# Optimization experiments

Measured on AMD Instinct MI355X. Metric: run time of the kernel, lower is better.

Reference implementation:

```python
import jax, jax.numpy as jnp
import numpy as np

N_NODES = 100000
N_EDGES = 1600000
IN_FEATS = 64
NUM_CLASSES = 64


def setup_inputs() -> dict:
    key = jax.random.key(0)
    k1, k2, k3, k4, k5, k6 = jax.random.split(key, 6)
    in_feat = jax.random.normal(k1, (N_NODES, IN_FEATS), dtype=jnp.float32)
    src = jax.random.randint(k2, (N_EDGES,), 0, N_NODES, dtype=jnp.int32)
    dst = jax.random.randint(k3, (N_EDGES,), 0, N_NODES, dtype=jnp.int32)
    scale = 1.0 / np.sqrt(IN_FEATS)
    W_self = jax.random.normal(k4, (IN_FEATS, NUM_CLASSES), dtype=jnp.float32) * scale
    W_neigh = jax.random.normal(k5, (IN_FEATS, NUM_CLASSES), dtype=jnp.float32) * scale
    bias = jax.random.normal(k6, (NUM_CLASSES,), dtype=jnp.float32) * 0.01
    return {"in_feat": in_feat, "src": src, "dst": dst,
            "W_self": W_self, "W_neigh": W_neigh, "bias": bias}


def reference(in_feat, src, dst, W_self, W_neigh, bias):
    # SAGEConv with 'mean' aggregator (DGL semantics):
    #   h_neigh[v] = mean over incoming edges (u->v) of in_feat[u]; 0 if no in-edges
    #   out = fc_self(x) + fc_neigh(h_neigh) + bias, then sigmoid
    n = in_feat.shape[0]
    msg = in_feat[src]                                            # [E, F] gather
    agg = jax.ops.segment_sum(msg, dst, num_segments=n)           # [N, F]
    deg = jax.ops.segment_sum(jnp.ones((src.shape[0],), jnp.float32), dst,
                              num_segments=n)                     # [N]
    h_neigh = agg / jnp.maximum(deg, 1.0)[:, None]                # mean, 0 for isolated
    out = in_feat @ W_self + h_neigh @ W_neigh + bias
    return jax.nn.sigmoid(out)
```

## Files before the change

kernel.cpp:

```cpp
#include <hip/hip_runtime.h>


constexpr int NN = 100000;
constexpr int NE = 1600000;
constexpr int F  = 64;
constexpr int RB = 256;
constexpr int NB = (NN + RB - 1) / RB;
constexpr int CH = 8192;
constexpr int PB = (NE + CH - 1) / CH;
constexpr int CAP = 2048;

typedef short bf16x8 __attribute__((ext_vector_type(8)));
typedef float f32x4  __attribute__((ext_vector_type(4)));
typedef float f32x2  __attribute__((ext_vector_type(2)));
typedef unsigned short u16;
typedef u16 u16x8 __attribute__((ext_vector_type(8)));

__device__ __forceinline__ u16 f2bf(float f) {
    unsigned u = __float_as_uint(f);
    unsigned r = (u + 0x7FFF + ((u >> 16) & 1)) >> 16;
    return (u16)r;
}

__global__ __launch_bounds__(256) void k_prep(const float* __restrict__ x,
                                              const float* __restrict__ Ws,
                                              const float* __restrict__ Wn,
                                              unsigned char* __restrict__ x8,
                                              u16* __restrict__ xb,
                                              u16* __restrict__ Bt) {
    const int i = blockIdx.x * 256 + threadIdx.x;
    if (i < NN * F / 8) {
        const int o = i * 8;
        float4 a = *(const float4*)&x[o];
        float4 b = *(const float4*)&x[o + 4];
        int lo = 0, hi = 0;
        lo = __builtin_amdgcn_cvt_pk_fp8_f32(a.x, a.y, lo, false);
        lo = __builtin_amdgcn_cvt_pk_fp8_f32(a.z, a.w, lo, true);
        hi = __builtin_amdgcn_cvt_pk_fp8_f32(b.x, b.y, hi, false);
        hi = __builtin_amdgcn_cvt_pk_fp8_f32(b.z, b.w, hi, true);
        *(int2*)&x8[o] = make_int2(lo, hi);
        u16x8 r;
        r[0] = f2bf(a.x); r[1] = f2bf(a.y); r[2] = f2bf(a.z); r[3] = f2bf(a.w);
        r[4] = f2bf(b.x); r[5] = f2bf(b.y); r[6] = f2bf(b.z); r[7] = f2bf(b.w);
        *(u16x8*)&xb[o] = r;
    } else if (i < NN * F / 8 + 1024) {
        const int j  = i - NN * F / 8;
        const int n  = j >> 4;
        const int kb = (j & 15) * 8;
        u16x8 r;
#pragma unroll
        for (int jj = 0; jj < 8; ++jj) {
            const int kk = kb + jj;
            const float w = (kk < 64) ? Ws[kk * 64 + n] : Wn[(kk - 64) * 64 + n];
            r[jj] = f2bf(w);
        }
        *(u16x8*)&Bt[n * 128 + kb] = r;
    }
}

__global__ __launch_bounds__(256) void k_hist(const int* __restrict__ dst,
                                              int* __restrict__ gcount) {
    __shared__ int h[NB];
    for (int i = threadIdx.x; i < NB; i += 256) h[i] = 0;
    __syncthreads();
    const int b0  = blockIdx.x * CH;
    const int end = min(b0 + CH, NE);
    for (int i = b0 + threadIdx.x * 4; i < end; i += 1024) {
        int4 d = *(const int4*)&dst[i];
        atomicAdd(&h[d.x >> 8], 1);
        atomicAdd(&h[d.y >> 8], 1);
        atomicAdd(&h[d.z >> 8], 1);
        atomicAdd(&h[d.w >> 8], 1);
    }
    __syncthreads();
    for (int i = threadIdx.x; i < NB; i += 256)
        if (h[i]) atomicAdd(&gcount[i], h[i]);
}

__global__ __launch_bounds__(512) void k_scan(const int* __restrict__ gcount,
                                              int* __restrict__ basep,
                                              int* __restrict__ cursor) {
    __shared__ int tmp[512];
    const int t = threadIdx.x;
    int val = (t < NB) ? gcount[t] : 0;
    tmp[t] = val;
    __syncthreads();
    int s = val;
    for (int o = 1; o < 512; o <<= 1) {
        int add = (t >= o) ? tmp[t - o] : 0;
        __syncthreads();
        s += add;
        tmp[t] = s;
        __syncthreads();
    }
    if (t < NB) {
        basep[t]  = s - val;
        cursor[t] = s - val;
    }
}

__global__ __launch_bounds__(512) void k_part(const int* __restrict__ src,
                                              const int* __restrict__ dst,
                                              int* __restrict__ cursor,
                                              unsigned* __restrict__ packed) {
    __shared__ unsigned stage[CH];
    __shared__ unsigned short bkt[CH];
    __shared__ int hist[NB], lscan[NB], lcur[NB], gpos[NB];
    __shared__ int tmp[512];

    const int t   = threadIdx.x;
    const int b0  = blockIdx.x * CH;
    const int cnt = min(CH, NE - b0);

    for (int i = t; i < NB; i += 512) hist[i] = 0;
    __syncthreads();

    int4 sv[4], dv[4];
#pragma unroll
    for (int j = 0; j < 4; ++j) {
        const int idx = j * 2048 + t * 4;
        if (idx < cnt) {
            sv[j] = *(const int4*)&src[b0 + idx];
            dv[j] = *(const int4*)&dst[b0 + idx];
            atomicAdd(&hist[dv[j].x >> 8], 1);
            atomicAdd(&hist[dv[j].y >> 8], 1);
            atomicAdd(&hist[dv[j].z >> 8], 1);
            atomicAdd(&hist[dv[j].w >> 8], 1);
        }
    }
    __syncthreads();

    int val = (t < NB) ? hist[t] : 0;
    tmp[t] = val;
    __syncthreads();
    int s = val;
    for (int o = 1; o < 512; o <<= 1) {
        int add = (t >= o) ? tmp[t - o] : 0;
        __syncthreads();
        s += add;
        tmp[t] = s;
        __syncthreads();
    }
    if (t < NB) {
        lscan[t] = s - val;
        lcur[t]  = s - val;
        gpos[t]  = val ? atomicAdd(&cursor[t], val) : 0;
    }
    __syncthreads();

#pragma unroll
    for (int j = 0; j < 4; ++j) {
        const int idx = j * 2048 + t * 4;
        if (idx < cnt) {
            const int ss[4] = {sv[j].x, sv[j].y, sv[j].z, sv[j].w};
            const int dd[4] = {dv[j].x, dv[j].y, dv[j].z, dv[j].w};
#pragma unroll
            for (int q = 0; q < 4; ++q) {
                const int b = dd[q] >> 8;
                const int p = atomicAdd(&lcur[b], 1);
                stage[p] = ((unsigned)(dd[q] & 255) << 17) | (unsigned)ss[q];
                bkt[p]   = (unsigned short)b;
            }
        }
    }
    __syncthreads();

    for (int i = t; i < cnt; i += 512) {
        const int b = bkt[i];
        packed[gpos[b] + (i - lscan[b])] = stage[i];
    }
}

__device__ __forceinline__ void acc8pk(f32x2& a0, f32x2& a1, f32x2& a2, f32x2& a3,
                                       int2 qq) {
#if __has_builtin(__builtin_amdgcn_cvt_pk_f32_fp8)
    a0 += __builtin_amdgcn_cvt_pk_f32_fp8(qq.x, false);
    a1 += __builtin_amdgcn_cvt_pk_f32_fp8(qq.x, true);
    a2 += __builtin_amdgcn_cvt_pk_f32_fp8(qq.y, false);
    a3 += __builtin_amdgcn_cvt_pk_f32_fp8(qq.y, true);
#else
    a0[0] += __builtin_amdgcn_cvt_f32_fp8(qq.x, 0);
    a0[1] += __builtin_amdgcn_cvt_f32_fp8(qq.x, 1);
    a1[0] += __builtin_amdgcn_cvt_f32_fp8(qq.x, 2);
    a1[1] += __builtin_amdgcn_cvt_f32_fp8(qq.x, 3);
    a2[0] += __builtin_amdgcn_cvt_f32_fp8(qq.y, 0);
    a2[1] += __builtin_amdgcn_cvt_f32_fp8(qq.y, 1);
    a3[0] += __builtin_amdgcn_cvt_f32_fp8(qq.y, 2);
    a3[1] += __builtin_amdgcn_cvt_f32_fp8(qq.y, 3);
#endif
}

__global__ __launch_bounds__(512) void k_fused(
    const unsigned char* __restrict__ x8, const u16* __restrict__ xb,
    const unsigned* __restrict__ packed, const int* __restrict__ basep,
    const u16* __restrict__ Bt, const float* __restrict__ bias,
    float* __restrict__ out)
{
    __shared__ u16 At[64 * 128];
    __shared__ unsigned stage[CAP];
    __shared__ int hist[64], cur[64], exar[64];

    const int blk  = blockIdx.x;
    const int base = blk * 64;
    const int bu   = blk >> 2;
    const int qq   = blk & 3;
    const int t    = threadIdx.x;
    const int nv   = min(64, NN - base);

    const int e0 = basep[bu];
    const int e1 = (bu == NB - 1) ? NE : basep[bu + 1];
    const int m  = e1 - e0;

    if (t < 64) hist[t] = 0;
    __syncthreads();

    for (int i = t; i < m; i += 512) {
        const unsigned p  = packed[e0 + i];
        const unsigned dl = p >> 17;
        if ((int)(dl >> 6) == qq) atomicAdd(&hist[dl & 63], 1);
    }
    __syncthreads();

    if (t < 64) {
        const int val = hist[t];
        int s = val;
#pragma unroll
        for (int o = 1; o < 64; o <<= 1) {
            const int nsh = __shfl_up(s, o);
            if (t >= o) s += nsh;
        }
        cur[t]  = s - val;
        exar[t] = s - val;
    }
    __syncthreads();

    for (int i = t; i < m; i += 512) {
        const unsigned p  = packed[e0 + i];
        const unsigned dl = p >> 17;
        if ((int)(dl >> 6) == qq) {
            const int pos = atomicAdd(&cur[dl & 63], 1);
            if (pos < CAP) stage[pos] = p & 0x1FFFFu;
        }
    }
    __syncthreads();

    const int r  = t >> 3;
    const int cg = t & 7;
    if (r < nv) {
        const int dg = hist[r];
        const int s0 = exar[r];
        f32x2 a0 = {0.f, 0.f}, a1 = a0, a2 = a0, a3 = a0;
        int e = 0;
        for (; e + 4 <= dg; e += 4) {
            const int i0 = stage[s0 + e + 0];
            const int i1 = stage[s0 + e + 1];
            const int i2 = stage[s0 + e + 2];
            const int i3 = stage[s0 + e + 3];
            int2 q0 = *(const int2*)&x8[(size_t)i0 * F + cg * 8];
            int2 q1 = *(const int2*)&x8[(size_t)i1 * F + cg * 8];
            int2 q2 = *(const int2*)&x8[(size_t)i2 * F + cg * 8];
            int2 q3 = *(const int2*)&x8[(size_t)i3 * F + cg * 8];
            acc8pk(a0, a1, a2, a3, q0);
            acc8pk(a0, a1, a2, a3, q1);
            acc8pk(a0, a1, a2, a3, q2);
            acc8pk(a0, a1, a2, a3, q3);
        }
        for (; e < dg; ++e) {
            int2 q = *(const int2*)&x8[(size_t)stage[s0 + e] * F + cg * 8];
            acc8pk(a0, a1, a2, a3, q);
        }
        const float inv = 1.0f / fmaxf((float)dg, 1.0f);

        u16x8 hb;
        hb[0] = f2bf(a0[0] * inv); hb[1] = f2bf(a0[1] * inv);
        hb[2] = f2bf(a1[0] * inv); hb[3] = f2bf(a1[1] * inv);
        hb[4] = f2bf(a2[0] * inv); hb[5] = f2bf(a2[1] * inv);
        hb[6] = f2bf(a3[0] * inv); hb[7] = f2bf(a3[1] * inv);
        const int bh = (8 + cg) ^ (r & 15);
        *(u16x8*)&At[r * 128 + bh * 8] = hb;

        const int bx = cg ^ (r & 15);
        *(u16x8*)&At[r * 128 + bx * 8] = *(const u16x8*)&xb[(size_t)(base + r) * F + cg * 8];
    }
    __syncthreads();

    const int w    = t >> 6;
    const int lane = t & 63;
    const int tr   = w >> 1;
    if (tr * 16 >= nv) return;
    const int nh   = w & 1;
    const int r16  = lane & 15;
    const int kg   = lane >> 4;

    bf16x8 bf[4][2];
#pragma unroll
    for (int t4 = 0; t4 < 4; ++t4)
#pragma unroll
        for (int uu = 0; uu < 2; ++uu) {
            const int n = (nh * 2 + uu) * 16 + r16;
            bf[t4][uu] = *(const bf16x8*)&Bt[n * 128 + t4 * 32 + kg * 8];
        }
    const float b0 = bias[(nh * 2 + 0) * 16 + r16];
    const float b1 = bias[(nh * 2 + 1) * 16 + r16];

    const int row = tr * 16 + r16;
    bf16x8 a[4];
#pragma unroll
    for (int t4 = 0; t4 < 4; ++t4) {
        const int blk16 = (t4 * 4 + kg) ^ (row & 15);
        a[t4] = *(const bf16x8*)&At[row * 128 + blk16 * 8];
    }

    f32x4 c0 = {0.f, 0.f, 0.f, 0.f}, c1 = c0;
    c0 = __builtin_amdgcn_mfma_f32_16x16x32_bf16(a[0], bf[0][0], c0, 0, 0, 0);
    c0 = __builtin_amdgcn_mfma_f32_16x16x32_bf16(a[1], bf[1][0], c0, 0, 0, 0);
    c0 = __builtin_amdgcn_mfma_f32_16x16x32_bf16(a[2], bf[2][0], c0, 0, 0, 0);
    c0 = __builtin_amdgcn_mfma_f32_16x16x32_bf16(a[3], bf[3][0], c0, 0, 0, 0);
    c1 = __builtin_amdgcn_mfma_f32_16x16x32_bf16(a[0], bf[0][1], c1, 0, 0, 0);
    c1 = __builtin_amdgcn_mfma_f32_16x16x32_bf16(a[1], bf[1][1], c1, 0, 0, 0);
    c1 = __builtin_amdgcn_mfma_f32_16x16x32_bf16(a[2], bf[2][1], c1, 0, 0, 0);
    c1 = __builtin_amdgcn_mfma_f32_16x16x32_bf16(a[3], bf[3][1], c1, 0, 0, 0);

    float* orow = out + (size_t)(base + tr * 16) * 64;
#pragma unroll
    for (int rr = 0; rr < 4; ++rr) {
        const int ro = (kg * 4 + rr) * 64;
        orow[ro + (nh * 2 + 0) * 16 + r16] = 1.0f / (1.0f + __expf(-(c0[rr] + b0)));
        orow[ro + (nh * 2 + 1) * 16 + r16] = 1.0f / (1.0f + __expf(-(c1[rr] + b1)));
    }
}

extern "C" void kernel_launch(void* const* d_in, const int* in_sizes, int n_in,
                              void* d_out, int out_size, void* d_ws, size_t ws_size,
                              hipStream_t stream) {
    const float* x    = (const float*)d_in[0];
    const int*   src  = (const int*)d_in[1];
    const int*   dst  = (const int*)d_in[2];
    const float* Ws   = (const float*)d_in[3];
    const float* Wn   = (const float*)d_in[4];
    const float* bias = (const float*)d_in[5];
    float* out = (float*)d_out;

    unsigned char* x8 = (unsigned char*)d_ws;
    u16* xb     = (u16*)(x8 + (size_t)NN * F);
    u16* Bt     = xb + (size_t)NN * F;
    int* gcount = (int*)(Bt + 64 * 128);
    int* basep  = gcount + NB;
    int* cursor = basep + NB;
    unsigned* packed = (unsigned*)(cursor + NB);

    hipMemsetAsync(gcount, 0, (size_t)NB * sizeof(int), stream);

    k_prep <<<(NN * F / 8 + 1024 + 255) / 256, 256, 0, stream>>>(x, Ws, Wn, x8, xb, Bt);
    k_hist <<<PB, 256, 0, stream>>>(dst, gcount);
    k_scan <<<1, 512, 0, stream>>>(gcount, basep, cursor);
    k_part <<<PB, 512, 0, stream>>>(src, dst, cursor, packed);

    k_fused<<<(NN + 63) / 64, 512, 0, stream>>>(x8, xb, packed, basep, Bt, bias, out);
}
```

Before: 87.74 us.

## Aggregate neighbours via edge-parallel LDS fixed-point atomics instead of per-row CSR

Replaces the histogram, scan and per-destination sort inside the fused kernel with one compaction pass into shared memory. The gather is then done edge-parallel: each 16-lane group handles one edge and adds its decoded fp8 features into a shared int accumulator using fixed-point atomicAdd. This removes a pass over the packed edges and the per-row load imbalance that comes from varying degree. In exchange it adds many LDS atomics and quantizes sums to 16.16 fixed point, which may cost accuracy.

```diff
diff --git a/kernel.cpp b/kernel.cpp
--- a/kernel.cpp
+++ b/kernel.cpp
@@ -9,6 +9,7 @@
 constexpr int CH = 8192;
 constexpr int PB = (NE + CH - 1) / CH;
 constexpr int CAP = 2048;
+constexpr int AST = 68;
 
 typedef short bf16x8 __attribute__((ext_vector_type(8)));
 typedef float f32x4  __attribute__((ext_vector_type(4)));
@@ -20,6 +21,19 @@
     unsigned u = __float_as_uint(f);
     unsigned r = (u + 0x7FFF + ((u >> 16) & 1)) >> 16;
     return (u16)r;
+}
+
+__device__ __forceinline__ void dec4(int q, float* v) {
+#if __has_builtin(__builtin_amdgcn_cvt_pk_f32_fp8)
+    f32x2 lo = __builtin_amdgcn_cvt_pk_f32_fp8(q, false);
+    f32x2 hi = __builtin_amdgcn_cvt_pk_f32_fp8(q, true);
+    v[0] = lo[0]; v[1] = lo[1]; v[2] = hi[0]; v[3] = hi[1];
+#else
+    v[0] = __builtin_amdgcn_cvt_f32_fp8(q, 0);
+    v[1] = __builtin_amdgcn_cvt_f32_fp8(q, 1);
+    v[2] = __builtin_amdgcn_cvt_f32_fp8(q, 2);
+    v[3] = __builtin_amdgcn_cvt_f32_fp8(q, 3);
+#endif
 }
 
 __global__ __launch_bounds__(256) void k_prep(const float* __restrict__ x,
@@ -171,25 +185,6 @@
     }
 }
 
-__device__ __forceinline__ void acc8pk(f32x2& a0, f32x2& a1, f32x2& a2, f32x2& a3,
-                                       int2 qq) {
-#if __has_builtin(__builtin_amdgcn_cvt_pk_f32_fp8)
-    a0 += __builtin_amdgcn_cvt_pk_f32_fp8(qq.x, false);
-    a1 += __builtin_amdgcn_cvt_pk_f32_fp8(qq.x, true);
-    a2 += __builtin_amdgcn_cvt_pk_f32_fp8(qq.y, false);
-    a3 += __builtin_amdgcn_cvt_pk_f32_fp8(qq.y, true);
-#else
-    a0[0] += __builtin_amdgcn_cvt_f32_fp8(qq.x, 0);
-    a0[1] += __builtin_amdgcn_cvt_f32_fp8(qq.x, 1);
-    a1[0] += __builtin_amdgcn_cvt_f32_fp8(qq.x, 2);
-    a1[1] += __builtin_amdgcn_cvt_f32_fp8(qq.x, 3);
-    a2[0] += __builtin_amdgcn_cvt_f32_fp8(qq.y, 0);
-    a2[1] += __builtin_amdgcn_cvt_f32_fp8(qq.y, 1);
-    a3[0] += __builtin_amdgcn_cvt_f32_fp8(qq.y, 2);
-    a3[1] += __builtin_amdgcn_cvt_f32_fp8(qq.y, 3);
-#endif
-}
-
 __global__ __launch_bounds__(512) void k_fused(
     const unsigned char* __restrict__ x8, const u16* __restrict__ xb,
     const unsigned* __restrict__ packed, const int* __restrict__ basep,
@@ -197,8 +192,10 @@
     float* __restrict__ out)
 {
     __shared__ u16 At[64 * 128];
+    __shared__ int agg[64 * AST];
     __shared__ unsigned stage[CAP];
-    __shared__ int hist[64], cur[64], exar[64];
+    __shared__ int deg[64];
+    __shared__ int scnt;
 
     const int blk  = blockIdx.x;
     const int base = blk * 64;
@@ -211,35 +208,40 @@
     const int e1 = (bu == NB - 1) ? NE : basep[bu + 1];
     const int m  = e1 - e0;
 
-    if (t < 64) hist[t] = 0;
+    for (int i = t; i < 64 * AST; i += 512) agg[i] = 0;
+    if (t < 64) deg[t] = 0;
+    if (t == 0) scnt = 0;
     __syncthreads();
 
     for (int i = t; i < m; i += 512) {
-        const unsigned p  = packed[e0 + i];
-        const unsigned dl = p >> 17;
-        if ((int)(dl >> 6) == qq) atomicAdd(&hist[dl & 63], 1);
-    }
-    __syncthreads();
-
-    if (t < 64) {
-        const int val = hist[t];
-        int s = val;
-#pragma unroll
-        for (int o = 1; o < 64; o <<= 1) {
-            const int nsh = __shfl_up(s, o);
-            if (t >= o) s += nsh;
-        }
-        cur[t]  = s - val;
-        exar[t] = s - val;
-    }
-    __syncthreads();
-
-    for (int i = t; i < m; i += 512) {
-        const unsigned p  = packed[e0 + i];
-        const unsigned dl = p >> 17;
-        if ((int)(dl >> 6) == qq) {
-            const int pos = atomicAdd(&cur[dl & 63], 1);
-            if (pos < CAP) stage[pos] = p & 0x1FFFFu;
+        const unsigned p = packed[e0 + i];
+        if ((int)(p >> 23) == qq) {
+            const int pos = atomicAdd(&scnt, 1);
+            if (pos < CAP) stage[pos] = p;
+        }
+    }
+    __syncthreads();
+    const int ns = min(scnt, CAP);
+
+    const int w    = t >> 6;
+    const int lane = t & 63;
+    const int eidx = lane >> 4;
+    const int l16  = lane & 15;
+    for (int g = w * 4; g < ns; g += 32) {
+        const int e = g + eidx;
+        if (e < ns) {
+            const unsigned p = stage[e];
+            const int r = (int)((p >> 17) & 63);
+            const int s = (int)(p & 0x1FFFFu);
+            const int q = *(const int*)&x8[(size_t)s * F + l16 * 4];
+            float v[4];
+            dec4(q, v);
+            const int ab = r * AST + l16 * 4;
+            atomicAdd(&agg[ab + 0], __float2int_rn(v[0] * 65536.f));
+            atomicAdd(&agg[ab + 1], __float2int_rn(v[1] * 65536.f));
+            atomicAdd(&agg[ab + 2], __float2int_rn(v[2] * 65536.f));
+            atomicAdd(&agg[ab + 3], __float2int_rn(v[3] * 65536.f));
+            if (l16 == 0) atomicAdd(&deg[r], 1);
         }
     }
     __syncthreads();
@@ -247,35 +249,11 @@
     const int r  = t >> 3;
     const int cg = t & 7;
     if (r < nv) {
-        const int dg = hist[r];
-        const int s0 = exar[r];
-        f32x2 a0 = {0.f, 0.f}, a1 = a0, a2 = a0, a3 = a0;
-        int e = 0;
-        for (; e + 4 <= dg; e += 4) {
-            const int i0 = stage[s0 + e + 0];
-            const int i1 = stage[s0 + e + 1];
-            const int i2 = stage[s0 + e + 2];
-            const int i3 = stage[s0 + e + 3];
-            int2 q0 = *(const int2*)&x8[(size_t)i0 * F + cg * 8];
-            int2 q1 = *(const int2*)&x8[(size_t)i1 * F + cg * 8];
-            int2 q2 = *(const int2*)&x8[(size_t)i2 * F + cg * 8];
-            int2 q3 = *(const int2*)&x8[(size_t)i3 * F + cg * 8];
-            acc8pk(a0, a1, a2, a3, q0);
-            acc8pk(a0, a1, a2, a3, q1);
-            acc8pk(a0, a1, a2, a3, q2);
-            acc8pk(a0, a1, a2, a3, q3);
-        }
-        for (; e < dg; ++e) {
-            int2 q = *(const int2*)&x8[(size_t)stage[s0 + e] * F + cg * 8];
-            acc8pk(a0, a1, a2, a3, q);
-        }
-        const float inv = 1.0f / fmaxf((float)dg, 1.0f);
-
+        const float inv = (1.0f / 65536.f) / fmaxf((float)deg[r], 1.0f);
         u16x8 hb;
-        hb[0] = f2bf(a0[0] * inv); hb[1] = f2bf(a0[1] * inv);
-        hb[2] = f2bf(a1[0] * inv); hb[3] = f2bf(a1[1] * inv);
-        hb[4] = f2bf(a2[0] * inv); hb[5] = f2bf(a2[1] * inv);
-        hb[6] = f2bf(a3[0] * inv); hb[7] = f2bf(a3[1] * inv);
+#pragma unroll
+        for (int j = 0; j < 8; ++j)
+            hb[j] = f2bf((float)agg[r * AST + cg * 8 + j] * inv);
         const int bh = (8 + cg) ^ (r & 15);
         *(u16x8*)&At[r * 128 + bh * 8] = hb;
 
@@ -284,13 +262,11 @@
     }
     __syncthreads();
 
-    const int w    = t >> 6;
-    const int lane = t & 63;
-    const int tr   = w >> 1;
+    const int tr = w >> 1;
     if (tr * 16 >= nv) return;
-    const int nh   = w & 1;
-    const int r16  = lane & 15;
-    const int kg   = lane >> 4;
+    const int nh  = w & 1;
+    const int r16 = lane & 15;
+    const int kg  = lane >> 4;
 
     bf16x8 bf[4][2];
 #pragma unroll
```

Result: slower. 115.1 us (+31.2%).

## Merge prep, histogram and scan into one kernel; halve bucket rereads in fused

Applied to the files above, without the earlier changes.

Folds the feature-conversion, destination histogram and global prefix scan into one launch: the last histogram block, detected through an atomic completion counter, performs the scan. This removes two kernel launches. The fused aggregation kernel now handles 128 nodes per block instead of 64, so each 256-node bucket's packed edge list is read by two blocks rather than four, and it keeps the edges in registers between the histogram and scatter passes instead of reading them twice. The risks are more register pressure from the 12-entry edge buffer, a larger shared staging area, and two sequential 64-row passes per block.

```diff
diff --git a/kernel.cpp b/kernel.cpp
--- a/kernel.cpp
+++ b/kernel.cpp
@@ -8,7 +8,9 @@
 constexpr int NB = (NN + RB - 1) / RB;
 constexpr int CH = 8192;
 constexpr int PB = (NE + CH - 1) / CH;
-constexpr int CAP = 2048;
+constexpr int PREPB = (NN * F / 8 + 1024 + 255) / 256;
+constexpr int SCAP = 3072;
+constexpr int NP = 12;
 
 typedef short bf16x8 __attribute__((ext_vector_type(8)));
 typedef float f32x4  __attribute__((ext_vector_type(4)));
@@ -20,155 +22,6 @@
     unsigned u = __float_as_uint(f);
     unsigned r = (u + 0x7FFF + ((u >> 16) & 1)) >> 16;
     return (u16)r;
-}
-
-__global__ __launch_bounds__(256) void k_prep(const float* __restrict__ x,
-                                              const float* __restrict__ Ws,
-                                              const float* __restrict__ Wn,
-                                              unsigned char* __restrict__ x8,
-                                              u16* __restrict__ xb,
-                                              u16* __restrict__ Bt) {
-    const int i = blockIdx.x * 256 + threadIdx.x;
-    if (i < NN * F / 8) {
-        const int o = i * 8;
-        float4 a = *(const float4*)&x[o];
-        float4 b = *(const float4*)&x[o + 4];
-        int lo = 0, hi = 0;
-        lo = __builtin_amdgcn_cvt_pk_fp8_f32(a.x, a.y, lo, false);
-        lo = __builtin_amdgcn_cvt_pk_fp8_f32(a.z, a.w, lo, true);
-        hi = __builtin_amdgcn_cvt_pk_fp8_f32(b.x, b.y, hi, false);
-        hi = __builtin_amdgcn_cvt_pk_fp8_f32(b.z, b.w, hi, true);
-        *(int2*)&x8[o] = make_int2(lo, hi);
-        u16x8 r;
-        r[0] = f2bf(a.x); r[1] = f2bf(a.y); r[2] = f2bf(a.z); r[3] = f2bf(a.w);
-        r[4] = f2bf(b.x); r[5] = f2bf(b.y); r[6] = f2bf(b.z); r[7] = f2bf(b.w);
-        *(u16x8*)&xb[o] = r;
-    } else if (i < NN * F / 8 + 1024) {
-        const int j  = i - NN * F / 8;
-        const int n  = j >> 4;
-        const int kb = (j & 15) * 8;
-        u16x8 r;
-#pragma unroll
-        for (int jj = 0; jj < 8; ++jj) {
-            const int kk = kb + jj;
-            const float w = (kk < 64) ? Ws[kk * 64 + n] : Wn[(kk - 64) * 64 + n];
-            r[jj] = f2bf(w);
-        }
-        *(u16x8*)&Bt[n * 128 + kb] = r;
-    }
-}
-
-__global__ __launch_bounds__(256) void k_hist(const int* __restrict__ dst,
-                                              int* __restrict__ gcount) {
-    __shared__ int h[NB];
-    for (int i = threadIdx.x; i < NB; i += 256) h[i] = 0;
-    __syncthreads();
-    const int b0  = blockIdx.x * CH;
-    const int end = min(b0 + CH, NE);
-    for (int i = b0 + threadIdx.x * 4; i < end; i += 1024) {
-        int4 d = *(const int4*)&dst[i];
-        atomicAdd(&h[d.x >> 8], 1);
-        atomicAdd(&h[d.y >> 8], 1);
-        atomicAdd(&h[d.z >> 8], 1);
-        atomicAdd(&h[d.w >> 8], 1);
-    }
-    __syncthreads();
-    for (int i = threadIdx.x; i < NB; i += 256)
-        if (h[i]) atomicAdd(&gcount[i], h[i]);
-}
-
-__global__ __launch_bounds__(512) void k_scan(const int* __restrict__ gcount,
-                                              int* __restrict__ basep,
-                                              int* __restrict__ cursor) {
-    __shared__ int tmp[512];
-    const int t = threadIdx.x;
-    int val = (t < NB) ? gcount[t] : 0;
-    tmp[t] = val;
-    __syncthreads();
-    int s = val;
-    for (int o = 1; o < 512; o <<= 1) {
-        int add = (t >= o) ? tmp[t - o] : 0;
-        __syncthreads();
-        s += add;
-        tmp[t] = s;
-        __syncthreads();
-    }
-    if (t < NB) {
-        basep[t]  = s - val;
-        cursor[t] = s - val;
-    }
-}
-
-__global__ __launch_bounds__(512) void k_part(const int* __restrict__ src,
-                                              const int* __restrict__ dst,
-                                              int* __restrict__ cursor,
-                                              unsigned* __restrict__ packed) {
-    __shared__ unsigned stage[CH];
-    __shared__ unsigned short bkt[CH];
-    __shared__ int hist[NB], lscan[NB], lcur[NB], gpos[NB];
-    __shared__ int tmp[512];
-
-    const int t   = threadIdx.x;
-    const int b0  = blockIdx.x * CH;
-    const int cnt = min(CH, NE - b0);
-
-    for (int i = t; i < NB; i += 512) hist[i] = 0;
-    __syncthreads();
-
-    int4 sv[4], dv[4];
-#pragma unroll
-    for (int j = 0; j < 4; ++j) {
-        const int idx = j * 2048 + t * 4;
-        if (idx < cnt) {
-            sv[j] = *(const int4*)&src[b0 + idx];
-            dv[j] = *(const int4*)&dst[b0 + idx];
-            atomicAdd(&hist[dv[j].x >> 8], 1);
-            atomicAdd(&hist[dv[j].y >> 8], 1);
-            atomicAdd(&hist[dv[j].z >> 8], 1);
-            atomicAdd(&hist[dv[j].w >> 8], 1);
-        }
-    }
-    __syncthreads();
-
-    int val = (t < NB) ? hist[t] : 0;
-    tmp[t] = val;
-    __syncthreads();
-    int s = val;
-    for (int o = 1; o < 512; o <<= 1) {
-        int add = (t >= o) ? tmp[t - o] : 0;
-        __syncthreads();
-        s += add;
-        tmp[t] = s;
-        __syncthreads();
-    }
-    if (t < NB) {
-        lscan[t] = s - val;
-        lcur[t]  = s - val;
-        gpos[t]  = val ? atomicAdd(&cursor[t], val) : 0;
-    }
-    __syncthreads();
-
-#pragma unroll
-    for (int j = 0; j < 4; ++j) {
-        const int idx = j * 2048 + t * 4;
-        if (idx < cnt) {
-            const int ss[4] = {sv[j].x, sv[j].y, sv[j].z, sv[j].w};
-            const int dd[4] = {dv[j].x, dv[j].y, dv[j].z, dv[j].w};
-#pragma unroll
-            for (int q = 0; q < 4; ++q) {
-                const int b = dd[q] >> 8;
-                const int p = atomicAdd(&lcur[b], 1);
-                stage[p] = ((unsigned)(dd[q] & 255) << 17) | (unsigned)ss[q];
-                bkt[p]   = (unsigned short)b;
-            }
-        }
-    }
-    __syncthreads();
-
-    for (int i = t; i < cnt; i += 512) {
-        const int b = bkt[i];
-        packed[gpos[b] + (i - lscan[b])] = stage[i];
-    }
 }
 
 __device__ __forceinline__ void acc8pk(f32x2& a0, f32x2& a1, f32x2& a2, f32x2& a3,
@@ -190,6 +43,168 @@
 #endif
 }
 
+__global__ __launch_bounds__(256) void k_prep_hist(
+    const float* __restrict__ x, const float* __restrict__ Ws,
+    const float* __restrict__ Wn, const int* __restrict__ dst,
+    unsigned char* __restrict__ x8, u16* __restrict__ xb, u16* __restrict__ Bt,
+    int* __restrict__ gcount, int* __restrict__ donecnt,
+    int* __restrict__ basep, int* __restrict__ cursor)
+{
+    const int bid = blockIdx.x;
+    const int t   = threadIdx.x;
+
+    if (bid < PREPB) {
+        const int i = bid * 256 + t;
+        if (i < NN * F / 8) {
+            const int o = i * 8;
+            float4 a = *(const float4*)&x[o];
+            float4 b = *(const float4*)&x[o + 4];
+            int lo = 0, hi = 0;
+            lo = __builtin_amdgcn_cvt_pk_fp8_f32(a.x, a.y, lo, false);
+            lo = __builtin_amdgcn_cvt_pk_fp8_f32(a.z, a.w, lo, true);
+            hi = __builtin_amdgcn_cvt_pk_fp8_f32(b.x, b.y, hi, false);
+            hi = __builtin_amdgcn_cvt_pk_fp8_f32(b.z, b.w, hi, true);
+            *(int2*)&x8[o] = make_int2(lo, hi);
+            u16x8 r;
+            r[0] = f2bf(a.x); r[1] = f2bf(a.y); r[2] = f2bf(a.z); r[3] = f2bf(a.w);
+            r[4] = f2bf(b.x); r[5] = f2bf(b.y); r[6] = f2bf(b.z); r[7] = f2bf(b.w);
+            *(u16x8*)&xb[o] = r;
+        } else if (i < NN * F / 8 + 1024) {
+            const int j  = i - NN * F / 8;
+            const int n  = j >> 4;
+            const int kb = (j & 15) * 8;
+            u16x8 r;
+#pragma unroll
+            for (int jj = 0; jj < 8; ++jj) {
+                const int kk = kb + jj;
+                const float w = (kk < 64) ? Ws[kk * 64 + n] : Wn[(kk - 64) * 64 + n];
+                r[jj] = f2bf(w);
+            }
+            *(u16x8*)&Bt[n * 128 + kb] = r;
+        }
+        return;
+    }
+
+    __shared__ int h[NB];
+    __shared__ int lastflag;
+    for (int i = t; i < NB; i += 256) h[i] = 0;
+    __syncthreads();
+    const int hb  = bid - PREPB;
+    const int b0  = hb * CH;
+    const int end = min(b0 + CH, NE);
+    for (int i = b0 + t * 4; i < end; i += 1024) {
+        int4 d = *(const int4*)&dst[i];
+        atomicAdd(&h[d.x >> 8], 1);
+        atomicAdd(&h[d.y >> 8], 1);
+        atomicAdd(&h[d.z >> 8], 1);
+        atomicAdd(&h[d.w >> 8], 1);
+    }
+    __syncthreads();
+    for (int i = t; i < NB; i += 256)
+        if (h[i]) atomicAdd(&gcount[i], h[i]);
+
+    __threadfence();
+    if (t == 0) lastflag = (atomicAdd(donecnt, 1) == PB - 1);
+    __syncthreads();
+    if (!lastflag || t >= 64) return;
+
+    int v[7], pre[7], s = 0;
+#pragma unroll
+    for (int j = 0; j < 7; ++j) {
+        const int idx = t * 7 + j;
+        v[j] = (idx < NB) ? atomicAdd(&gcount[idx], 0) : 0;
+        pre[j] = s;
+        s += v[j];
+    }
+    int run = s;
+#pragma unroll
+    for (int o = 1; o < 64; o <<= 1) {
+        const int n = __shfl_up(run, o);
+        if (t >= o) run += n;
+    }
+    const int lbase = run - s;
+#pragma unroll
+    for (int j = 0; j < 7; ++j) {
+        const int idx = t * 7 + j;
+        if (idx < NB) {
+            basep[idx]  = lbase + pre[j];
+            cursor[idx] = lbase + pre[j];
+        }
+    }
+}
+
+__global__ __launch_bounds__(512) void k_part(const int* __restrict__ src,
+                                              const int* __restrict__ dst,
+                                              int* __restrict__ cursor,
+                                              unsigned* __restrict__ packed) {
+    __shared__ unsigned stage[CH];
+    __shared__ unsigned short bkt[CH];
+    __shared__ int hist[NB], lscan[NB], lcur[NB], gpos[NB];
+    __shared__ int tmp[512];
+
+    const int t   = threadIdx.x;
+    const int b0  = blockIdx.x * CH;
+    const int cnt = min(CH, NE - b0);
+
+    for (int i = t; i < NB; i += 512) hist[i] = 0;
+    __syncthreads();
+
+    int4 sv[4], dv[4];
+#pragma unroll
+    for (int j = 0; j < 4; ++j) {
+        const int idx = j * 2048 + t * 4;
+        if (idx < cnt) {
+            sv[j] = *(const int4*)&src[b0 + idx];
+            dv[j] = *(const int4*)&dst[b0 + idx];
+            atomicAdd(&hist[dv[j].x >> 8], 1);
+            atomicAdd(&hist[dv[j].y >> 8], 1);
+            atomicAdd(&hist[dv[j].z >> 8], 1);
+            atomicAdd(&hist[dv[j].w >> 8], 1);
+        }
+    }
+    __syncthreads();
+
+    int val = (t < NB) ? hist[t] : 0;
+    tmp[t] = val;
+    __syncthreads();
+    int s = val;
+    for (int o = 1; o < 512; o <<= 1) {
+        int add = (t >= o) ? tmp[t - o] : 0;
+        __syncthreads();
+        s += add;
+        tmp[t] = s;
+        __syncthreads();
+    }
+    if (t < NB) {
+        lscan[t] = s - val;
+        lcur[t]  = s - val;
+        gpos[t]  = val ? atomicAdd(&cursor[t], val) : 0;
+    }
+    __syncthreads();
+
+#pragma unroll
+    for (int j = 0; j < 4; ++j) {
+        const int idx = j * 2048 + t * 4;
+        if (idx < cnt) {
+            const int ss[4] = {sv[j].x, sv[j].y, sv[j].z, sv[j].w};
+            const int dd[4] = {dv[j].x, dv[j].y, dv[j].z, dv[j].w};
+#pragma unroll
+            for (int q = 0; q < 4; ++q) {
+                const int b = dd[q] >> 8;
+                const int p = atomicAdd(&lcur[b], 1);
+                stage[p] = ((unsigned)(dd[q] & 255) << 17) | (unsigned)ss[q];
+                bkt[p]   = (unsigned short)b;
+            }
+        }
+    }
+    __syncthreads();
+
+    for (int i = t; i < cnt; i += 512) {
+        const int b = bkt[i];
+        packed[gpos[b] + (i - lscan[b])] = stage[i];
+    }
+}
+
 __global__ __launch_bounds__(512) void k_fused(
     const unsigned char* __restrict__ x8, const u16* __restrict__ xb,
     const unsigned* __restrict__ packed, const int* __restrict__ basep,
@@ -197,136 +212,148 @@
     float* __restrict__ out)
 {
     __shared__ u16 At[64 * 128];
-    __shared__ unsigned stage[CAP];
-    __shared__ int hist[64], cur[64], exar[64];
+    __shared__ unsigned stage[SCAP];
+    __shared__ int hist[128], cur[128], exar[128];
 
     const int blk  = blockIdx.x;
-    const int base = blk * 64;
-    const int bu   = blk >> 2;
-    const int qq   = blk & 3;
+    const int bu   = blk >> 1;
+    const int hh   = blk & 1;
+    const int base = bu * RB + hh * 128;
     const int t    = threadIdx.x;
-    const int nv   = min(64, NN - base);
 
     const int e0 = basep[bu];
     const int e1 = (bu == NB - 1) ? NE : basep[bu + 1];
     const int m  = e1 - e0;
 
-    if (t < 64) hist[t] = 0;
-    __syncthreads();
-
-    for (int i = t; i < m; i += 512) {
-        const unsigned p  = packed[e0 + i];
-        const unsigned dl = p >> 17;
-        if ((int)(dl >> 6) == qq) atomicAdd(&hist[dl & 63], 1);
+    if (t < 128) hist[t] = 0;
+    __syncthreads();
+
+    unsigned pv[NP];
+#pragma unroll
+    for (int j = 0; j < NP; ++j) {
+        const int i = t + j * 512;
+        unsigned p = 0xFFFFFFFFu;
+        if (i < m) p = packed[e0 + i];
+        pv[j] = p;
+        if (p != 0xFFFFFFFFu && ((p >> 24) & 1u) == (unsigned)hh)
+            atomicAdd(&hist[(p >> 17) & 127], 1);
     }
     __syncthreads();
 
     if (t < 64) {
-        const int val = hist[t];
-        int s = val;
+        const int v0 = hist[2 * t], v1 = hist[2 * t + 1];
+        const int sv = v0 + v1;
+        int run = sv;
 #pragma unroll
         for (int o = 1; o < 64; o <<= 1) {
-            const int nsh = __shfl_up(s, o);
-            if (t >= o) s += nsh;
-        }
-        cur[t]  = s - val;
-        exar[t] = s - val;
-    }
-    __syncthreads();
-
-    for (int i = t; i < m; i += 512) {
-        const unsigned p  = packed[e0 + i];
-        const unsigned dl = p >> 17;
-        if ((int)(dl >> 6) == qq) {
-            const int pos = atomicAdd(&cur[dl & 63], 1);
-            if (pos < CAP) stage[pos] = p & 0x1FFFFu;
-        }
-    }
-    __syncthreads();
-
-    const int r  = t >> 3;
-    const int cg = t & 7;
-    if (r < nv) {
-        const int dg = hist[r];
-        const int s0 = exar[r];
-        f32x2 a0 = {0.f, 0.f}, a1 = a0, a2 = a0, a3 = a0;
-        int e = 0;
-        for (; e + 4 <= dg; e += 4) {
-            const int i0 = stage[s0 + e + 0];
-            const int i1 = stage[s0 + e + 1];
-            const int i2 = stage[s0 + e + 2];
-            const int i3 = stage[s0 + e + 3];
-            int2 q0 = *(const int2*)&x8[(size_t)i0 * F + cg * 8];
-            int2 q1 = *(const int2*)&x8[(size_t)i1 * F + cg * 8];
-            int2 q2 = *(const int2*)&x8[(size_t)i2 * F + cg * 8];
-            int2 q3 = *(const int2*)&x8[(size_t)i3 * F + cg * 8];
-            acc8pk(a0, a1, a2, a3, q0);
-            acc8pk(a0, a1, a2, a3, q1);
-            acc8pk(a0, a1, a2, a3, q2);
-            acc8pk(a0, a1, a2, a3, q3);
-        }
-        for (; e < dg; ++e) {
-            int2 q = *(const int2*)&x8[(size_t)stage[s0 + e] * F + cg * 8];
-            acc8pk(a0, a1, a2, a3, q);
-        }
-        const float inv = 1.0f / fmaxf((float)dg, 1.0f);
-
-        u16x8 hb;
-        hb[0] = f2bf(a0[0] * inv); hb[1] = f2bf(a0[1] * inv);
-        hb[2] = f2bf(a1[0] * inv); hb[3] = f2bf(a1[1] * inv);
-        hb[4] = f2bf(a2[0] * inv); hb[5] = f2bf(a2[1] * inv);
-        hb[6] = f2bf(a3[0] * inv); hb[7] = f2bf(a3[1] * inv);
-        const int bh = (8 + cg) ^ (r & 15);
-        *(u16x8*)&At[r * 128 + bh * 8] = hb;
-
-        const int bx = cg ^ (r & 15);
-        *(u16x8*)&At[r * 128 + bx * 8] = *(const u16x8*)&xb[(size_t)(base + r) * F + cg * 8];
-    }
-    __syncthreads();
-
+            const int n = __shfl_up(run, o);
+            if (t >= o) run += n;
+        }
+        const int b0 = run - sv;
+        exar[2 * t] = b0;      exar[2 * t + 1] = b0 + v0;
+        cur[2 * t]  = b0;      cur[2 * t + 1]  = b0 + v0;
+    }
+    __syncthreads();
+
+#pragma unroll
+    for (int j = 0; j < NP; ++j) {
+        const unsigned p = pv[j];
+        if (p != 0xFFFFFFFFu && ((p >> 24) & 1u) == (unsigned)hh) {
+            const int pos = atomicAdd(&cur[(p >> 17) & 127], 1);
+            if (pos < SCAP) stage[pos] = p & 0x1FFFFu;
+        }
+    }
+    __syncthreads();
+
+    const int r    = t >> 3;
+    const int cg   = t & 7;
     const int w    = t >> 6;
     const int lane = t & 63;
     const int tr   = w >> 1;
-    if (tr * 16 >= nv) return;
     const int nh   = w & 1;
     const int r16  = lane & 15;
     const int kg   = lane >> 4;
 
-    bf16x8 bf[4][2];
-#pragma unroll
-    for (int t4 = 0; t4 < 4; ++t4)
-#pragma unroll
-        for (int uu = 0; uu < 2; ++uu) {
-            const int n = (nh * 2 + uu) * 16 + r16;
-            bf[t4][uu] = *(const bf16x8*)&Bt[n * 128 + t4 * 32 + kg * 8];
-        }
-    const float b0 = bias[(nh * 2 + 0) * 16 + r16];
-    const float b1 = bias[(nh * 2 + 1) * 16 + r16];
-
-    const int row = tr * 16 + r16;
-    bf16x8 a[4];
-#pragma unroll
-    for (int t4 = 0; t4 < 4; ++t4) {
-        const int blk16 = (t4 * 4 + kg) ^ (row & 15);
-        a[t4] = *(const bf16x8*)&At[row * 128 + blk16 * 8];
-    }
-
-    f32x4 c0 = {0.f, 0.f, 0.f, 0.f}, c1 = c0;
-    c0 = __builtin_amdgcn_mfma_f32_16x16x32_bf16(a[0], bf[0][0], c0, 0, 0, 0);
-    c0 = __builtin_amdgcn_mfma_f32_16x16x32_bf16(a[1], bf[1][0], c0, 0, 0, 0);
-    c0 = __builtin_amdgcn_mfma_f32_16x16x32_bf16(a[2], bf[2][0], c0, 0, 0, 0);
-    c0 = __builtin_amdgcn_mfma_f32_16x16x32_bf16(a[3], bf[3][0], c0, 0, 0, 0);
-    c1 = __builtin_amdgcn_mfma_f32_16x16x32_bf16(a[0], bf[0][1], c1, 0, 0, 0);
-    c1 = __builtin_amdgcn_mfma_f32_16x16x32_bf16(a[1], bf[1][1], c1, 0, 0, 0);
-    c1 = __builtin_amdgcn_mfma_f32_16x16x32_bf16(a[2], bf[2][1], c1, 0, 0, 0);
-    c1 = __builtin_amdgcn_mfma_f32_16x16x32_bf16(a[3], bf[3][1], c1, 0, 0, 0);
-
-    float* orow = out + (size_t)(base + tr * 16) * 64;
-#pragma unroll
-    for (int rr = 0; rr < 4; ++rr) {
-        const int ro = (kg * 4 + rr) * 64;
-        orow[ro + (nh * 2 + 0) * 16 + r16] = 1.0f / (1.0f + __expf(-(c0[rr] + b0)));
-        orow[ro + (nh * 2 + 1) * 16 + r16] = 1.0f / (1.0f + __expf(-(c1[rr] + b1)));
+    for (int q = 0; q < 2; ++q) {
+        const int nb64 = base + q * 64;
+        const int nv_r = min(64, NN - nb64);
+
+        if (nv_r > 0 && r < nv_r) {
+            const int ln = q * 64 + r;
+            const int dg = hist[ln];
+            const int s0 = exar[ln];
+            f32x2 a0 = {0.f, 0.f}, a1 = a0, a2 = a0, a3 = a0;
+            int e = 0;
+            for (; e + 4 <= dg; e += 4) {
+                const int i0 = stage[s0 + e + 0];
+                const int i1 = stage[s0 + e + 1];
+                const int i2 = stage[s0 + e + 2];
+                const int i3 = stage[s0 + e + 3];
+                int2 q0 = *(const int2*)&x8[(size_t)i0 * F + cg * 8];
+                int2 q1 = *(const int2*)&x8[(size_t)i1 * F + cg * 8];
+                int2 q2 = *(const int2*)&x8[(size_t)i2 * F + cg * 8];
+                int2 q3 = *(const int2*)&x8[(size_t)i3 * F + cg * 8];
+                acc8pk(a0, a1, a2, a3, q0);
+                acc8pk(a0, a1, a2, a3, q1);
+                acc8pk(a0, a1, a2, a3, q2);
+                acc8pk(a0, a1, a2, a3, q3);
+            }
+            for (; e < dg; ++e) {
+                int2 qv = *(const int2*)&x8[(size_t)stage[s0 + e] * F + cg * 8];
+                acc8pk(a0, a1, a2, a3, qv);
+            }
+            const float inv = 1.0f / fmaxf((float)dg, 1.0f);
+            u16x8 hbv;
+            hbv[0] = f2bf(a0[0] * inv); hbv[1] = f2bf(a0[1] * inv);
+            hbv[2] = f2bf(a1[0] * inv); hbv[3] = f2bf(a1[1] * inv);
+            hbv[4] = f2bf(a2[0] * inv); hbv[5] = f2bf(a2[1] * inv);
+            hbv[6] = f2bf(a3[0] * inv); hbv[7] = f2bf(a3[1] * inv);
+            const int bh = (8 + cg) ^ (r & 15);
+            *(u16x8*)&At[r * 128 + bh * 8] = hbv;
+            const int bx = cg ^ (r & 15);
+            *(u16x8*)&At[r * 128 + bx * 8] = *(const u16x8*)&xb[(size_t)(nb64 + r) * F + cg * 8];
+        }
+        __syncthreads();
+
+        if (nv_r > 0 && tr * 16 < nv_r) {
+            bf16x8 bfr[4][2];
+#pragma unroll
+            for (int t4 = 0; t4 < 4; ++t4)
+#pragma unroll
+                for (int uu = 0; uu < 2; ++uu) {
+                    const int n = (nh * 2 + uu) * 16 + r16;
+                    bfr[t4][uu] = *(const bf16x8*)&Bt[n * 128 + t4 * 32 + kg * 8];
+                }
+            const float b0 = bias[(nh * 2 + 0) * 16 + r16];
+            const float b1 = bias[(nh * 2 + 1) * 16 + r16];
+
+            const int row = tr * 16 + r16;
+            bf16x8 a[4];
+#pragma unroll
+            for (int t4 = 0; t4 < 4; ++t4) {
+                const int blk16 = (t4 * 4 + kg) ^ (row & 15);
+                a[t4] = *(const bf16x8*)&At[row * 128 + blk16 * 8];
+            }
+
+            f32x4 c0 = {0.f, 0.f, 0.f, 0.f}, c1 = c0;
+            c0 = __builtin_amdgcn_mfma_f32_16x16x32_bf16(a[0], bfr[0][0], c0, 0, 0, 0);
+            c0 = __builtin_amdgcn_mfma_f32_16x16x32_bf16(a[1], bfr[1][0], c0, 0, 0, 0);
+            c0 = __builtin_amdgcn_mfma_f32_16x16x32_bf16(a[2], bfr[2][0], c0, 0, 0, 0);
+            c0 = __builtin_amdgcn_mfma_f32_16x16x32_bf16(a[3], bfr[3][0], c0, 0, 0, 0);
+            c1 = __builtin_amdgcn_mfma_f32_16x16x32_bf16(a[0], bfr[0][1], c1, 0, 0, 0);
+            c1 = __builtin_amdgcn_mfma_f32_16x16x32_bf16(a[1], bfr[1][1], c1, 0, 0, 0);
+            c1 = __builtin_amdgcn_mfma_f32_16x16x32_bf16(a[2], bfr[2][1], c1, 0, 0, 0);
+            c1 = __builtin_amdgcn_mfma_f32_16x16x32_bf16(a[3], bfr[3][1], c1, 0, 0, 0);
+
+            float* orow = out + (size_t)(nb64 + tr * 16) * 64;
+#pragma unroll
+            for (int rr = 0; rr < 4; ++rr) {
+                const int ro = (kg * 4 + rr) * 64;
+                orow[ro + (nh * 2 + 0) * 16 + r16] = 1.0f / (1.0f + __expf(-(c0[rr] + b0)));
+                orow[ro + (nh * 2 + 1) * 16 + r16] = 1.0f / (1.0f + __expf(-(c1[rr] + b1)));
+            }
+        }
+        __syncthreads();
     }
 }
 
@@ -341,20 +368,19 @@
     const float* bias = (const float*)d_in[5];
     float* out = (float*)d_out;
 
-    unsigned char* x8 = (unsigned char*)d_ws;
-    u16* xb     = (u16*)(x8 + (size_t)NN * F);
-    u16* Bt     = xb + (size_t)NN * F;
-    int* gcount = (int*)(Bt + 64 * 128);
-    int* basep  = gcount + NB;
-    int* cursor = basep + NB;
+    int* gcount  = (int*)d_ws;
+    int* donecnt = gcount + NB;
+    int* basep   = donecnt + 1;
+    int* cursor  = basep + NB;
     unsigned* packed = (unsigned*)(cursor + NB);
-
-    hipMemsetAsync(gcount, 0, (size_t)NB * sizeof(int), stream);
-
-    k_prep <<<(NN * F / 8 + 1024 + 255) / 256, 256, 0, stream>>>(x, Ws, Wn, x8, xb, Bt);
-    k_hist <<<PB, 256, 0, stream>>>(dst, gcount);
-    k_scan <<<1, 512, 0, stream>>>(gcount, basep, cursor);
+    unsigned char* x8 = (unsigned char*)(packed + NE);
+    u16* xb = (u16*)(x8 + (size_t)NN * F);
+    u16* Bt = xb + (size_t)NN * F;
+
+    hipMemsetAsync(gcount, 0, (size_t)(NB + 1) * sizeof(int), stream);
+
+    k_prep_hist<<<PREPB + PB, 256, 0, stream>>>(x, Ws, Wn, dst, x8, xb, Bt,
+                                                gcount, donecnt, basep, cursor);
     k_part <<<PB, 512, 0, stream>>>(src, dst, cursor, packed);
-
-    k_fused<<<(NN + 63) / 64, 512, 0, stream>>>(x8, xb, packed, basep, Bt, bias, out);
-}
+    k_fused<<<(NN + 127) / 128, 512, 0, stream>>>(x8, xb, packed, basep, Bt, bias, out);
+}
```

After: 102.8 us. 17.1% more time.
